# Performance work log

Hardware: AMD Instinct MI355X
Metric: run time of the kernel (lower is better)

Reference implementation:

```python
import jax, jax.numpy as jnp
import numpy as np

B, C, H, W = 4, 512, 64, 64
C8 = C // 8


def setup_inputs() -> dict:
    key = jax.random.key(0)
    ks = jax.random.split(key, 5)
    s1 = 1.0 / np.sqrt(C)
    return {
        "feat_map": jax.random.normal(ks[0], (B, C, H, W), jnp.float32),
        "w1": jax.random.normal(ks[1], (C8, C), jnp.float32) * s1,
        "b1": jnp.zeros((C8,), jnp.float32),
        "w2": jax.random.normal(ks[2], (C8, C), jnp.float32) * s1,
        "b2": jnp.zeros((C8,), jnp.float32),
        "w3": jax.random.normal(ks[3], (C, C), jnp.float32) * s1,
        "b3": jnp.zeros((C,), jnp.float32),
        "gamma": jax.random.normal(ks[4], (1,), jnp.float32) * 0.1,
    }


def reference(feat_map, w1, b1, w2, b2, w3, b3, gamma):
    b, c, h, w = feat_map.shape
    n = h * w
    x = feat_map.reshape(b, c, n)  # [B,C,N]
    # 1x1 convs are channel-mixing GEMMs
    q = jnp.einsum('kc,bcn->bnk', w1, x) + b1[None, None, :]   # [B,N,C8]
    k = jnp.einsum('kc,bcn->bkn', w2, x) + b2[None, :, None]   # [B,C8,N]
    v = jnp.einsum('dc,bcn->bdn', w3, x) + b3[None, :, None]   # [B,C,N]
    relation = jnp.einsum('bik,bkj->bij', q, k)                # [B,N,N]
    attn = jax.nn.softmax(relation, axis=-1)                   # softmax over keys j
    # feat_refine[b,c,i] = sum_j v[b,c,j] * attn[b,i,j]
    refine = jnp.einsum('bdj,bij->bdi', v, attn)               # [B,C,N]
    out = gamma[0] * refine.reshape(b, c, h, w) + feat_map
    return out
```

## Files before the change

kernel.cpp:

```cpp
#include <hip/hip_runtime.h>
#include <hip/hip_bf16.h>

typedef __attribute__((ext_vector_type(8))) short bf16x8_t;
typedef __attribute__((ext_vector_type(4))) float f32x4_t;

#define B_   4
#define C_   512
#define N_   4096
#define NQK_ 128
#define NT_  128
#define NP_  64

typedef unsigned short ushort_t;

__device__ __forceinline__ ushort_t f2bf(float f) {
    union { float f; unsigned int u; } un; un.f = f;
    unsigned int r = un.u + 0x7FFF + ((un.u >> 16) & 1);
    return (ushort_t)(r >> 16);
}

__device__ __forceinline__ bf16x8_t load8(const ushort_t* p) {
    return *reinterpret_cast<const bf16x8_t*>(p);
}

__device__ __forceinline__ unsigned pk2(float lo, float hi) {
    return (unsigned)f2bf(lo) | ((unsigned)f2bf(hi) << 16);
}

#define GLL16(g, l) __builtin_amdgcn_global_load_lds( \
    (const __attribute__((address_space(1))) unsigned int*)(g), \
    (__attribute__((address_space(3))) unsigned int*)(l), 16, 0, 0)

__global__ __launch_bounds__(256) void transpose_cast_x(
        const float* __restrict__ x, ushort_t* __restrict__ Xt,
        const float* __restrict__ w1, const float* __restrict__ b1,
        const float* __restrict__ w2, const float* __restrict__ b2,
        const float* __restrict__ w3, const float* __restrict__ b3,
        ushort_t* __restrict__ Wb, float* __restrict__ bias_all) {
    if (blockIdx.z == 4) {
        int bid = blockIdx.y * 64 + blockIdx.x;
        int t0 = bid * 256 + threadIdx.x;
        for (int idx = t0; idx < 640 * 512 + 640; idx += 131072) {
            if (idx < 64 * 512) {
                Wb[idx] = f2bf(w1[idx]);
            } else if (idx < 128 * 512) {
                Wb[idx] = f2bf(w2[idx - 64 * 512]);
            } else if (idx < 640 * 512) {
                Wb[idx] = f2bf(w3[idx - 128 * 512]);
            } else {
                int i = idx - 640 * 512;
                bias_all[i] = (i < 64) ? b1[i] : (i < 128 ? b2[i - 64] : b3[i - 128]);
            }
        }
        return;
    }
    int b = blockIdx.z, c0 = blockIdx.y * 64, n0 = blockIdx.x * 64;
    int tid = threadIdx.x;
    __shared__ float t[64][65];
    const float* xb = x + ((size_t)b * C_ + c0) * N_ + n0;
    #pragma unroll
    for (int it = 0; it < 16; ++it) {
        int cl = it * 4 + (tid >> 6), nl = tid & 63;
        t[cl][nl] = xb[(size_t)cl * N_ + nl];
    }
    __syncthreads();
    #pragma unroll
    for (int it = 0; it < 16; ++it) {
        int nl = it * 4 + (tid >> 6), cl = tid & 63;
        Xt[((size_t)b * N_ + n0 + nl) * C_ + c0 + cl] = f2bf(t[cl][nl]);
    }
}

__global__ __launch_bounds__(256) void gemm_qkv_kernel(
        const ushort_t* __restrict__ Xt, const ushort_t* __restrict__ Wb,
        const float* __restrict__ bias, ushort_t* __restrict__ QK,
        ushort_t* __restrict__ V) {
    int sel = blockIdx.y;
    int n0 = blockIdx.x * 128;
    int tid = threadIdx.x;
    int l = tid & 63, w = tid >> 6;
    int wr = w >> 1, wc = w & 1;
    int lr = l & 15, lg = l >> 4;
    if (sel < 4) {
        int b = sel;
        const ushort_t* Xb = Xt + (size_t)b * N_ * C_;
        const ushort_t* ap = Xb + (size_t)(n0 + wr * 64 + lr) * 512 + lg * 8;
        const ushort_t* bp = Wb + (size_t)(wc * 64 + lr) * 512 + lg * 8;
        f32x4_t acc[4][4] = {};
        bf16x8_t a[4], bb[4];
        #pragma unroll
        for (int f = 0; f < 4; ++f) {
            a[f]  = load8(ap + (size_t)f * 16 * 512);
            bb[f] = load8(bp + (size_t)f * 16 * 512);
        }
        for (int kk = 0; kk < 512; kk += 32) {
            bf16x8_t na[4], nbb[4];
            if (kk + 32 < 512) {
                #pragma unroll
                for (int f = 0; f < 4; ++f) {
                    na[f]  = load8(ap + (size_t)f * 16 * 512 + kk + 32);
                    nbb[f] = load8(bp + (size_t)f * 16 * 512 + kk + 32);
                }
            }
            #pragma unroll
            for (int fi = 0; fi < 4; ++fi)
                #pragma unroll
                for (int fj = 0; fj < 4; ++fj)
                    acc[fi][fj] = __builtin_amdgcn_mfma_f32_16x16x32_bf16(
                        a[fi], bb[fj], acc[fi][fj], 0, 0, 0);
            if (kk + 32 < 512) {
                #pragma unroll
                for (int f = 0; f < 4; ++f) { a[f] = na[f]; bb[f] = nbb[f]; }
            }
        }
        #pragma unroll
        for (int fi = 0; fi < 4; ++fi)
            #pragma unroll
            for (int fj = 0; fj < 4; ++fj)
                #pragma unroll
                for (int r = 0; r < 4; ++r) {
                    int n = n0 + wr * 64 + fi * 16 + lg * 4 + r;
                    int col = wc * 64 + fj * 16 + lr;
                    QK[((size_t)b * N_ + n) * NQK_ + col] = f2bf(acc[fi][fj][r] + bias[col]);
                }
    } else {
        int m0 = ((sel - 4) & 3) * 128;
        int b  = (sel - 4) >> 2;
        const ushort_t* Xb = Xt + (size_t)b * N_ * C_;
        const ushort_t* Wv = Wb + 128 * 512;
        const ushort_t* ap = Wv + (size_t)(m0 + wr * 64 + lr) * 512 + lg * 8;
        const ushort_t* bp = Xb + (size_t)(n0 + wc * 64 + lr) * 512 + lg * 8;
        f32x4_t acc[4][4] = {};
        bf16x8_t a[4], bb[4];
        #pragma unroll
        for (int f = 0; f < 4; ++f) {
            a[f]  = load8(ap + (size_t)f * 16 * 512);
            bb[f] = load8(bp + (size_t)f * 16 * 512);
        }
        for (int kk = 0; kk < 512; kk += 32) {
            bf16x8_t na[4], nbb[4];
            if (kk + 32 < 512) {
                #pragma unroll
                for (int f = 0; f < 4; ++f) {
                    na[f]  = load8(ap + (size_t)f * 16 * 512 + kk + 32);
                    nbb[f] = load8(bp + (size_t)f * 16 * 512 + kk + 32);
                }
            }
            #pragma unroll
            for (int fi = 0; fi < 4; ++fi)
                #pragma unroll
                for (int fj = 0; fj < 4; ++fj)
                    acc[fi][fj] = __builtin_amdgcn_mfma_f32_16x16x32_bf16(
                        a[fi], bb[fj], acc[fi][fj], 0, 0, 0);
            if (kk + 32 < 512) {
                #pragma unroll
                for (int f = 0; f < 4; ++f) { a[f] = na[f]; bb[f] = nbb[f]; }
            }
        }
        #pragma unroll
        for (int fi = 0; fi < 4; ++fi)
            #pragma unroll
            for (int fj = 0; fj < 4; ++fj)
                #pragma unroll
                for (int r = 0; r < 4; ++r) {
                    int d = m0 + wr * 64 + fi * 16 + lg * 4 + r;
                    int n = n0 + wc * 64 + fj * 16 + lr;
                    V[((size_t)b * C_ + d) * N_ + n] = f2bf(acc[fi][fj][r] + bias[128 + d]);
                }
    }
}

__global__ __launch_bounds__(768, 3) void attn_kernel(
        const ushort_t* __restrict__ QK, const ushort_t* __restrict__ V,
        const float* __restrict__ feat, const float* __restrict__ gamma,
        float* __restrict__ out) {
    __shared__ ushort_t Vl[3][16384];
    __shared__ ushort_t Kl3[3][4096];
    __shared__ ushort_t Pl[2][4096];
    __shared__ float    fl[2][128];
    __shared__ __align__(16) unsigned flagl[2][8];
    __shared__ float    invl[64];

    int bid = blockIdx.x;
    int lid = (bid & 7) * 32 + (bid >> 3);
    int b  = lid >> 6;
    int i0 = (lid & 63) * 64;

    int tid = threadIdx.x;
    int l = tid & 63, w = tid >> 6;
    int lr = l & 15, lg = l >> 4;
    int ds = (w >= 4) ? (w - 4) : 0;

    const ushort_t* QKb = QK + (size_t)b * N_ * NQK_;
    const ushort_t* Vb  = V  + (size_t)b * C_ * N_;

    bf16x8_t qf0 = {}, qf1 = {};
    const ushort_t* ksrc = nullptr;
    float mreg = -1e30f, ssum = 0.0f;
    const int maskk = (lr & 7) << 4;
    if (w < 4) {
        qf0 = load8(QKb + (size_t)(i0 + w * 16 + lr) * NQK_ + lg * 8);
        qf1 = load8(QKb + (size_t)(i0 + w * 16 + lr) * NQK_ + 32 + lg * 8);
        int p = w * 1024 + l * 16;
        int o = p ^ (((p >> 7) & 7) << 4);
        ksrc = QKb + (size_t)(o >> 7) * NQK_ + 64 + ((o & 127) >> 1);
    }

    int cst = (l & 7) ^ (l >> 3);
    const ushort_t* vsrc = Vb + (size_t)(ds * 64 + 2 * (l >> 3) + (cst >> 2)) * N_
                              + (cst & 3) * 8;
    int c2 = ((lr & 1) * 4 + lg) ^ (lr >> 1);
    const int vread = ds * 2048 + (lr >> 1) * 64 + c2 * 8;
    f32x4_t acc[4][4] = {};

    if (w < 4) {
        GLL16(ksrc,                         &Kl3[0][w * 512]);
        GLL16(ksrc + (size_t)1 * 32 * NQK_, &Kl3[0][2048 + w * 512]);
        GLL16(ksrc + (size_t)2 * 32 * NQK_, &Kl3[1][w * 512]);
        GLL16(ksrc + (size_t)3 * 32 * NQK_, &Kl3[1][2048 + w * 512]);
        asm volatile("s_waitcnt vmcnt(2)" ::: "memory");
    } else {
        #pragma unroll
        for (int h = 0; h < 4; ++h)
            GLL16(vsrc + (size_t)h * 16 * N_,      &Vl[0][ds * 2048 + h * 512]);
        #pragma unroll
        for (int h = 0; h < 4; ++h)
            GLL16(vsrc + (size_t)h * 16 * N_ + 32, &Vl[1][ds * 2048 + h * 512]);
        #pragma unroll
        for (int h = 0; h < 4; ++h)
            GLL16(vsrc + (size_t)h * 16 * N_ + 64, &Vl[2][ds * 2048 + h * 512]);
    }
    asm volatile("" ::: "memory");
    __builtin_amdgcn_s_barrier();
    asm volatile("" ::: "memory");

#define SOFTMAX_WRITE(SO0, SO1, PM, TT)                                        \
    {                                                                          \
        float pmax = fmaxf(fmaxf(fmaxf(SO0[0],SO0[1]), fmaxf(SO0[2],SO0[3])),  \
                           fmaxf(fmaxf(SO1[0],SO1[1]), fmaxf(SO1[2],SO1[3]))); \
        pmax = fmaxf(pmax, __shfl_xor(pmax, 16));                              \
        pmax = fmaxf(pmax, __shfl_xor(pmax, 32));                              \
        bool anyneed = __any(pmax > mreg + 8.0f);                              \
        if (anyneed) {                                                         \
            float mn = fmaxf(mreg, pmax);                                      \
            float f_ = __expf(mreg - mn);                                      \
            mreg = mn; ssum *= f_;                                             \
            if (lg == 0) fl[PM][(TT) * 64 + w * 16 + lr] = f_;                 \
        }                                                                      \
        if (l == 0) flagl[PM][(TT) * 4 + w] = anyneed ? 1u : 0u;               \
        float e00 = __expf(SO0[0]-mreg), e01 = __expf(SO0[1]-mreg);            \
        float e02 = __expf(SO0[2]-mreg), e03 = __expf(SO0[3]-mreg);            \
        float e10 = __expf(SO1[0]-mreg), e11 = __expf(SO1[1]-mreg);            \
        float e12 = __expf(SO1[2]-mreg), e13 = __expf(SO1[3]-mreg);            \
        ssum += (e00+e01)+(e02+e03)+(e10+e11)+(e12+e13);    \
        int lt = lr + (lg >> 1) * 16;                                          \
        uint2 w0v; w0v.x = pk2(e00, e01); w0v.y = pk2(e02, e03);               \
        uint2 w1v; w1v.x = pk2(e10, e11); w1v.y = pk2(e12, e13);               \
        *reinterpret_cast<uint2*>(&Pl[PM][(TT)*2048 + w*512 + lt*8 + (lg&1)*4]) = w0v; \
        *reinterpret_cast<uint2*>(&Pl[PM][(TT)*2048 + w*512 + (lt+32)*8 + (lg&1)*4]) = w1v; \
    }

#define PVSTEP(PB, TT, VB, STJ, DOSTAGE)                                       \
    {                                                                          \
        bf16x8_t vf[4];                                                        \
        _Pragma("unroll") for (int dt = 0; dt < 4; ++dt)                       \
            vf[dt] = load8(&Vl[VB][vread + dt * 512]);                         \
        asm volatile("s_waitcnt lgkmcnt(0)" ::: "memory");                     \
        if (DOSTAGE) {                                                         \
            const ushort_t* vsT = vsrc + (STJ) * 32;                           \
            _Pragma("unroll") for (int h = 0; h < 4; ++h)                      \
                GLL16(vsT + (size_t)h * 16 * N_, &Vl[VB][ds * 2048 + h * 512]); \
        }                                                                      \
        uint4 fv = *reinterpret_cast<const uint4*>(&flagl[PB][(TT) * 4]);      \
        if ((int)__builtin_amdgcn_readfirstlane(fv.x)) {                       \
            float fq = fl[PB][(TT) * 64 + lr];                                 \
            _Pragma("unroll") for (int dt = 0; dt < 4; ++dt) acc[dt][0] *= fq; \
        }                                                                      \
        if ((int)__builtin_amdgcn_readfirstlane(fv.y)) {                       \
            float fq = fl[PB][(TT) * 64 + 16 + lr];                            \
            _Pragma("unroll") for (int dt = 0; dt < 4; ++dt) acc[dt][1] *= fq; \
        }                                                                      \
        if ((int)__builtin_amdgcn_readfirstlane(fv.z)) {                       \
            float fq = fl[PB][(TT) * 64 + 32 + lr];                            \
            _Pragma("unroll") for (int dt = 0; dt < 4; ++dt) acc[dt][2] *= fq; \
        }                                                                      \
        if ((int)__builtin_amdgcn_readfirstlane(fv.w)) {                       \
            float fq = fl[PB][(TT) * 64 + 48 + lr];                            \
            _Pragma("unroll") for (int dt = 0; dt < 4; ++dt) acc[dt][3] *= fq; \
        }                                                                      \
        _Pragma("unroll") for (int qt = 0; qt < 4; ++qt) {                     \
            bf16x8_t pa = load8(&Pl[PB][(TT) * 2048 + qt * 512 + l * 8]);      \
            _Pragma("unroll") for (int dt = 0; dt < 4; ++dt)                   \
                acc[dt][qt] = __builtin_amdgcn_mfma_f32_16x16x32_bf16(         \
                    vf[dt], pa, acc[dt][qt], 0, 0, 0);                         \
        }                                                                      \
    }

    for (int p = 0; p < NP_; ++p) {
        int pb = p % 3;
        if (w < 4) {
            if (p + 2 < NP_) {
                int pn = pb + 2; if (pn >= 3) pn -= 3;
                GLL16(ksrc + (size_t)(2 * p + 4) * 32 * NQK_, &Kl3[pn][w * 512]);
                GLL16(ksrc + (size_t)(2 * p + 5) * 32 * NQK_, &Kl3[pn][2048 + w * 512]);
            }
            const ushort_t* kbp = &Kl3[pb][0];
            bf16x8_t kf00, kf01, kf10, kf11;
            { int o = (lr << 7) + (lg << 4);              kf00 = load8(kbp + ((o ^ maskk) >> 1)); }
            { int o = (lr << 7) + 64 + (lg << 4);         kf01 = load8(kbp + ((o ^ maskk) >> 1)); }
            { int o = ((16 + lr) << 7) + (lg << 4);       kf10 = load8(kbp + ((o ^ maskk) >> 1)); }
            { int o = ((16 + lr) << 7) + 64 + (lg << 4);  kf11 = load8(kbp + ((o ^ maskk) >> 1)); }
            f32x4_t s00 = {0.f,0.f,0.f,0.f}, s01 = {0.f,0.f,0.f,0.f};
            s00 = __builtin_amdgcn_mfma_f32_16x16x32_bf16(kf00, qf0, s00, 0,0,0);
            s00 = __builtin_amdgcn_mfma_f32_16x16x32_bf16(kf01, qf1, s00, 0,0,0);
            s01 = __builtin_amdgcn_mfma_f32_16x16x32_bf16(kf10, qf0, s01, 0,0,0);
            s01 = __builtin_amdgcn_mfma_f32_16x16x32_bf16(kf11, qf1, s01, 0,0,0);
            const ushort_t* kbq = kbp + 2048;
            bf16x8_t kg00, kg01, kg10, kg11;
            { int o = (lr << 7) + (lg << 4);              kg00 = load8(kbq + ((o ^ maskk) >> 1)); }
            { int o = (lr << 7) + 64 + (lg << 4);         kg01 = load8(kbq + ((o ^ maskk) >> 1)); }
            { int o = ((16 + lr) << 7) + (lg << 4);       kg10 = load8(kbq + ((o ^ maskk) >> 1)); }
            { int o = ((16 + lr) << 7) + 64 + (lg << 4);  kg11 = load8(kbq + ((o ^ maskk) >> 1)); }
            f32x4_t s10 = {0.f,0.f,0.f,0.f}, s11 = {0.f,0.f,0.f,0.f};
            s10 = __builtin_amdgcn_mfma_f32_16x16x32_bf16(kg00, qf0, s10, 0,0,0);
            s10 = __builtin_amdgcn_mfma_f32_16x16x32_bf16(kg01, qf1, s10, 0,0,0);
            s11 = __builtin_amdgcn_mfma_f32_16x16x32_bf16(kg10, qf0, s11, 0,0,0);
            s11 = __builtin_amdgcn_mfma_f32_16x16x32_bf16(kg11, qf1, s11, 0,0,0);
            int bank = p & 1;
            SOFTMAX_WRITE(s00, s01, bank, 0)
            SOFTMAX_WRITE(s10, s11, bank, 1)
            asm volatile("s_waitcnt vmcnt(2) lgkmcnt(0)" ::: "memory");
        } else {
            if (p >= 1) {
                int pbk = (p - 1) & 1;
                int j0 = 2 * p - 2, j1 = 2 * p - 1;
                PVSTEP(pbk, 0, j0 % 3, j0 + 3, (j0 + 3 < NT_))
                PVSTEP(pbk, 1, j1 % 3, j1 + 3, (j1 + 3 < NT_))
            }
            asm volatile("s_waitcnt vmcnt(4)" ::: "memory");
        }
        asm volatile("" ::: "memory");
        __builtin_amdgcn_s_barrier();
        asm volatile("" ::: "memory");
    }

    if (w < 4) {
        ssum += __shfl_xor(ssum, 16);
        ssum += __shfl_xor(ssum, 32);
        if (lg == 0) invl[w * 16 + lr] = 1.0f / ssum;
        asm volatile("s_waitcnt lgkmcnt(0)" ::: "memory");
    } else {
        asm volatile("s_waitcnt vmcnt(0)" ::: "memory");
    }
    asm volatile("" ::: "memory");
    __builtin_amdgcn_s_barrier();
    asm volatile("" ::: "memory");

    if (w >= 4) {
        PVSTEP(1, 0, 0, 0, false)
        PVSTEP(1, 1, 1, 0, false)
        asm volatile("s_waitcnt lgkmcnt(0)" ::: "memory");

        float g = gamma[0];
        float iq0 = invl[lr], iq1 = invl[16 + lr], iq2 = invl[32 + lr], iq3 = invl[48 + lr];
        #pragma unroll
        for (int dt = 0; dt < 4; ++dt) {
            #pragma unroll
            for (int r = 0; r < 4; ++r) {
                size_t row = ((size_t)b * C_ + ds * 64 + dt * 16 + lg * 4 + r) * N_;
                size_t i0r = row + i0;
                { size_t idx = i0r + lr;      out[idx] = g * acc[dt][0][r] * iq0 + feat[idx]; }
                { size_t idx = i0r + 16 + lr; out[idx] = g * acc[dt][1][r] * iq1 + feat[idx]; }
                { size_t idx = i0r + 32 + lr; out[idx] = g * acc[dt][2][r] * iq2 + feat[idx]; }
                { size_t idx = i0r + 48 + lr; out[idx] = g * acc[dt][3][r] * iq3 + feat[idx]; }
            }
        }
    }
#undef PVSTEP
#undef SOFTMAX_WRITE
}

extern "C" void kernel_launch(void* const* d_in, const int* in_sizes, int n_in,
                              void* d_out, int out_size, void* d_ws, size_t ws_size,
                              hipStream_t stream) {
    const float* feat  = (const float*)d_in[0];
    const float* w1    = (const float*)d_in[1];
    const float* b1    = (const float*)d_in[2];
    const float* w2    = (const float*)d_in[3];
    const float* b2    = (const float*)d_in[4];
    const float* w3    = (const float*)d_in[5];
    const float* b3    = (const float*)d_in[6];
    const float* gamma = (const float*)d_in[7];
    float* out = (float*)d_out;

    char* ws = (char*)d_ws;
    ushort_t* Xt      = (ushort_t*)(ws);
    ushort_t* Wb      = (ushort_t*)(ws + 16777216);
    float*    biasAll = (float*)   (ws + 17432576);
    ushort_t* QKp     = (ushort_t*)(ws + 17435136);
    ushort_t* Vp      = (ushort_t*)(ws + 21629440);
    if (ws_size < 38406656) return;

    hipLaunchKernelGGL(transpose_cast_x, dim3(64, 8, 5), dim3(256), 0, stream,
                       feat, Xt, w1, b1, w2, b2, w3, b3, Wb, biasAll);
    hipLaunchKernelGGL(gemm_qkv_kernel, dim3(32, 20), dim3(256), 0, stream,
                       Xt, Wb, biasAll, QKp, Vp);
    hipLaunchKernelGGL(attn_kernel, dim3(256), dim3(768), 0, stream,
                       QKp, Vp, feat, gamma, out);
}
```

Before: 165.5 us.

## Load V fragments directly from global into registers instead of LDS ring

The PV-consumer waves no longer stage V tiles through a three-deep shared-memory ring. Each lane now loads its MFMA operand fragments straight from global memory into two register sets (A/B) that are double-buffered across softmax phases. This removes the large Vl shared array, the LDS reads and writes of V, and the explicit vmcnt and lgkmcnt waits around them, and it frees shared memory that could allow more blocks per CU. In exchange, global loads become narrow 64-byte row segments that are less well coalesced, and their latency must be hidden by a single loop iteration of lookahead.

```diff
diff --git a/kernel.cpp b/kernel.cpp
--- a/kernel.cpp
+++ b/kernel.cpp
@@ -174,7 +174,6 @@
         const ushort_t* __restrict__ QK, const ushort_t* __restrict__ V,
         const float* __restrict__ feat, const float* __restrict__ gamma,
         float* __restrict__ out) {
-    __shared__ ushort_t Vl[3][16384];
     __shared__ ushort_t Kl3[3][4096];
     __shared__ ushort_t Pl[2][4096];
     __shared__ float    fl[2][128];
@@ -206,11 +205,8 @@
         ksrc = QKb + (size_t)(o >> 7) * NQK_ + 64 + ((o & 127) >> 1);
     }
 
-    int cst = (l & 7) ^ (l >> 3);
-    const ushort_t* vsrc = Vb + (size_t)(ds * 64 + 2 * (l >> 3) + (cst >> 2)) * N_
-                              + (cst & 3) * 8;
-    int c2 = ((lr & 1) * 4 + lg) ^ (lr >> 1);
-    const int vread = ds * 2048 + (lr >> 1) * 64 + c2 * 8;
+    bf16x8_t vA0, vA1, vA2, vA3, vB0, vB1, vB2, vB3;
+    const ushort_t* vg = Vb + (size_t)(ds * 64 + lr) * N_ + lg * 8;
     f32x4_t acc[4][4] = {};
 
     if (w < 4) {
@@ -220,15 +216,16 @@
         GLL16(ksrc + (size_t)3 * 32 * NQK_, &Kl3[1][2048 + w * 512]);
         asm volatile("s_waitcnt vmcnt(2)" ::: "memory");
     } else {
-        #pragma unroll
-        for (int h = 0; h < 4; ++h)
-            GLL16(vsrc + (size_t)h * 16 * N_,      &Vl[0][ds * 2048 + h * 512]);
-        #pragma unroll
-        for (int h = 0; h < 4; ++h)
-            GLL16(vsrc + (size_t)h * 16 * N_ + 32, &Vl[1][ds * 2048 + h * 512]);
-        #pragma unroll
-        for (int h = 0; h < 4; ++h)
-            GLL16(vsrc + (size_t)h * 16 * N_ + 64, &Vl[2][ds * 2048 + h * 512]);
+        vA0 = load8(vg);
+        vA1 = load8(vg + (size_t)16 * N_);
+        vA2 = load8(vg + (size_t)32 * N_);
+        vA3 = load8(vg + (size_t)48 * N_);
+        vg += 32;
+        vB0 = load8(vg);
+        vB1 = load8(vg + (size_t)16 * N_);
+        vB2 = load8(vg + (size_t)32 * N_);
+        vB3 = load8(vg + (size_t)48 * N_);
+        vg += 32;
     }
     asm volatile("" ::: "memory");
     __builtin_amdgcn_s_barrier();
@@ -260,17 +257,8 @@
         *reinterpret_cast<uint2*>(&Pl[PM][(TT)*2048 + w*512 + (lt+32)*8 + (lg&1)*4]) = w1v; \
     }
 
-#define PVSTEP(PB, TT, VB, STJ, DOSTAGE)                                       \
+#define PVSTEP_R(PB, TT, V0, V1, V2, V3)                                       \
     {                                                                          \
-        bf16x8_t vf[4];                                                        \
-        _Pragma("unroll") for (int dt = 0; dt < 4; ++dt)                       \
-            vf[dt] = load8(&Vl[VB][vread + dt * 512]);                         \
-        asm volatile("s_waitcnt lgkmcnt(0)" ::: "memory");                     \
-        if (DOSTAGE) {                                                         \
-            const ushort_t* vsT = vsrc + (STJ) * 32;                           \
-            _Pragma("unroll") for (int h = 0; h < 4; ++h)                      \
-                GLL16(vsT + (size_t)h * 16 * N_, &Vl[VB][ds * 2048 + h * 512]); \
-        }                                                                      \
         uint4 fv = *reinterpret_cast<const uint4*>(&flagl[PB][(TT) * 4]);      \
         if ((int)__builtin_amdgcn_readfirstlane(fv.x)) {                       \
             float fq = fl[PB][(TT) * 64 + lr];                                 \
@@ -290,9 +278,14 @@
         }                                                                      \
         _Pragma("unroll") for (int qt = 0; qt < 4; ++qt) {                     \
             bf16x8_t pa = load8(&Pl[PB][(TT) * 2048 + qt * 512 + l * 8]);      \
-            _Pragma("unroll") for (int dt = 0; dt < 4; ++dt)                   \
-                acc[dt][qt] = __builtin_amdgcn_mfma_f32_16x16x32_bf16(         \
-                    vf[dt], pa, acc[dt][qt], 0, 0, 0);                         \
+            acc[0][qt] = __builtin_amdgcn_mfma_f32_16x16x32_bf16(              \
+                V0, pa, acc[0][qt], 0, 0, 0);                                  \
+            acc[1][qt] = __builtin_amdgcn_mfma_f32_16x16x32_bf16(              \
+                V1, pa, acc[1][qt], 0, 0, 0);                                  \
+            acc[2][qt] = __builtin_amdgcn_mfma_f32_16x16x32_bf16(              \
+                V2, pa, acc[2][qt], 0, 0, 0);                                  \
+            acc[3][qt] = __builtin_amdgcn_mfma_f32_16x16x32_bf16(              \
+                V3, pa, acc[3][qt], 0, 0, 0);                                  \
         }                                                                      \
     }
 
@@ -333,11 +326,19 @@
         } else {
             if (p >= 1) {
                 int pbk = (p - 1) & 1;
-                int j0 = 2 * p - 2, j1 = 2 * p - 1;
-                PVSTEP(pbk, 0, j0 % 3, j0 + 3, (j0 + 3 < NT_))
-                PVSTEP(pbk, 1, j1 % 3, j1 + 3, (j1 + 3 < NT_))
-            }
-            asm volatile("s_waitcnt vmcnt(4)" ::: "memory");
+                PVSTEP_R(pbk, 0, vA0, vA1, vA2, vA3)
+                vA0 = load8(vg);
+                vA1 = load8(vg + (size_t)16 * N_);
+                vA2 = load8(vg + (size_t)32 * N_);
+                vA3 = load8(vg + (size_t)48 * N_);
+                vg += 32;
+                PVSTEP_R(pbk, 1, vB0, vB1, vB2, vB3)
+                vB0 = load8(vg);
+                vB1 = load8(vg + (size_t)16 * N_);
+                vB2 = load8(vg + (size_t)32 * N_);
+                vB3 = load8(vg + (size_t)48 * N_);
+                vg += 32;
+            }
         }
         asm volatile("" ::: "memory");
         __builtin_amdgcn_s_barrier();
@@ -349,17 +350,14 @@
         ssum += __shfl_xor(ssum, 32);
         if (lg == 0) invl[w * 16 + lr] = 1.0f / ssum;
         asm volatile("s_waitcnt lgkmcnt(0)" ::: "memory");
-    } else {
-        asm volatile("s_waitcnt vmcnt(0)" ::: "memory");
     }
     asm volatile("" ::: "memory");
     __builtin_amdgcn_s_barrier();
     asm volatile("" ::: "memory");
 
     if (w >= 4) {
-        PVSTEP(1, 0, 0, 0, false)
-        PVSTEP(1, 1, 1, 0, false)
-        asm volatile("s_waitcnt lgkmcnt(0)" ::: "memory");
+        PVSTEP_R(1, 0, vA0, vA1, vA2, vA3)
+        PVSTEP_R(1, 1, vB0, vB1, vB2, vB3)
 
         float g = gamma[0];
         float iq0 = invl[lr], iq1 = invl[16 + lr], iq2 = invl[32 + lr], iq3 = invl[48 + lr];
@@ -376,7 +374,7 @@
             }
         }
     }
-#undef PVSTEP
+#undef PVSTEP_R
 #undef SOFTMAX_WRITE
 }
 
```

Result: slower. 189.0 us (+14.2%).
